# Optimization experiments

Hardware: AMD Instinct MI355X
Metric: run time of the kernel (lower is better)

Reference implementation:

```python
import jax, jax.numpy as jnp
import numpy as np
import math

T, N, P, H, E, S, R = 64, 1024, 256, 256, 512, 16, 16

def _sincos(n, d):
    pos = np.arange(n)[:, None].astype(np.float32)
    div = np.exp(np.arange(0, d, 2).astype(np.float32) * -(math.log(10000.0) / d))
    pe = np.zeros((n, d), np.float32)
    pe[:, 0::2] = np.sin(pos * div)
    pe[:, 1::2] = np.cos(pos * div)
    return jnp.asarray(pe)

def setup_inputs():
    key = jax.random.key(0)
    ks = iter(jax.random.split(key, 40))
    def w(shape, s=0.05):
        return jax.random.normal(next(ks), shape, jnp.float32) * s
    adj_seq = (jax.random.uniform(next(ks), (T, N, N)) < 0.05).astype(jnp.float32)
    return dict(
        adj_seq=adj_seq,
        pos_emb=_sincos(N, P),
        g1_Wm=w((P, H)), g1_bm=jnp.zeros((H,), jnp.float32),
        g1_Wq=w((H, H)), g1_Wk=w((H, H)), g1_gb=jnp.asarray(-1.0, jnp.float32),
        g1_Wu=w((P + H, H)), g1_bu=jnp.zeros((H,), jnp.float32),
        g1_lg=jnp.ones((H,), jnp.float32), g1_lb=jnp.zeros((H,), jnp.float32),
        g2_Wm=w((H, H)), g2_bm=jnp.zeros((H,), jnp.float32),
        g2_Wu=w((2 * H, H)), g2_bu=jnp.zeros((H,), jnp.float32),
        g2_lg=jnp.ones((H,), jnp.float32), g2_lb=jnp.zeros((H,), jnp.float32),
        m_lg=jnp.ones((H,), jnp.float32), m_lb=jnp.zeros((H,), jnp.float32),
        m_Win=w((H, 2 * E)), m_bin=jnp.zeros((2 * E,), jnp.float32),
        m_Wdelta=w((E, R)), m_bdelta=jnp.zeros((R,), jnp.float32),
        m_Wdt=w((R, E)), m_bdt=jnp.zeros((E,), jnp.float32),
        m_WB=w((E, S)), m_bB=jnp.zeros((S,), jnp.float32),
        m_WC=w((E, S)), m_bC=jnp.zeros((S,), jnp.float32),
        m_Alog=-jnp.exp(w((E, S), 0.1)),
        m_D=jnp.zeros((E,), jnp.float32),
        m_Wout=w((E, H)), m_bout=jnp.zeros((H,), jnp.float32),
    )

def _ln(x, g, b):
    mu = x.mean(-1, keepdims=True)
    v = ((x - mu) ** 2).mean(-1, keepdims=True)
    return (x - mu) / jnp.sqrt(v + 1e-5) * g + b

def reference(adj_seq, pos_emb, g1_Wm, g1_bm, g1_Wq, g1_Wk, g1_gb, g1_Wu, g1_bu,
              g1_lg, g1_lb, g2_Wm, g2_bm, g2_Wu, g2_bu, g2_lg, g2_lb,
              m_lg, m_lb, m_Win, m_bin, m_Wdelta, m_bdelta, m_Wdt, m_bdt,
              m_WB, m_bB, m_WC, m_bC, m_Alog, m_D, m_Wout, m_bout):
    scale = math.sqrt(H) * max(1.0, 1e-6)  # sqrt(d) * gate_temperature

    def encode(adj):  # adj: [N,N]
        msgs = pos_emb @ g1_Wm + g1_bm                 # [N,H]
        q = msgs @ g1_Wq
        k = msgs @ g1_Wk
        gates = jax.nn.sigmoid(q @ k.T / scale + g1_gb)
        agg = (gates * adj) @ msgs                     # gated aggregation
        x = _ln(jax.nn.relu(jnp.concatenate([pos_emb, agg], -1) @ g1_Wu + g1_bu), g1_lg, g1_lb)
        msgs2 = x @ g2_Wm + g2_bm
        agg2 = adj @ msgs2                             # ungated layer 2
        x = _ln(jax.nn.relu(jnp.concatenate([x, agg2], -1) @ g2_Wu + g2_bu), g2_lg, g2_lb)
        return x                                       # [N,H]

    seq = jax.vmap(encode)(adj_seq)                    # [T,N,H]
    x = seq.transpose(1, 0, 2)                         # [N,T,H] node-batched sequences

    # --- MambaBlock ---
    res = x
    xn = _ln(x, m_lg, m_lb)
    xp = xn @ m_Win + m_bin
    u, gate = jnp.split(xp, 2, axis=-1)                # [N,T,E] each
    u = jax.nn.silu(u)
    delta = jax.nn.softplus((u @ m_Wdelta + m_bdelta) @ m_Wdt + m_bdt)  # [N,T,E]
    Bm = u @ m_WB + m_bB                               # [N,T,S]
    Cm = u @ m_WC + m_bC                               # [N,T,S]
    A = -jnp.exp(m_Alog)                               # [E,S]

    def step(h, inp):
        u_t, d_t, B_t, C_t = inp                       # [N,E],[N,E],[N,S],[N,S]
        Ad = jnp.exp(d_t[:, :, None] * A[None])        # [N,E,S]
        h = Ad * h + d_t[:, :, None] * B_t[:, None, :] * u_t[:, :, None]
        y = jnp.einsum('ns,nes->ne', C_t, h)
        return h, y

    h0 = jnp.zeros((N, E, S), x.dtype)
    _, ys = jax.lax.scan(step, h0, (u.transpose(1, 0, 2), delta.transpose(1, 0, 2),
                                    Bm.transpose(1, 0, 2), Cm.transpose(1, 0, 2)))
    y = ys.transpose(1, 0, 2)                          # [N,T,E]
    y = (y + u * m_D) * jax.nn.silu(gate)
    out = y @ m_Wout + m_bout + res                    # [N,T,H]
    return out.transpose(1, 0, 2)                      # [T,N,H]
```

## Files before the change

### kernel.cpp

```cpp
#include <hip/hip_runtime.h>
#include <hip/hip_bf16.h>

typedef __hip_bfloat16 bf16;
typedef __attribute__((ext_vector_type(8))) short s16x8;
typedef __attribute__((ext_vector_type(4))) short s16x4;
typedef __attribute__((ext_vector_type(4))) float f32x4;

#define TT 64
#define NN_ 1024
#define EE 512

__device__ __forceinline__ float toF(float v) { return v; }
__device__ __forceinline__ float toF(bf16 v) { return __bfloat162float(v); }
__device__ __forceinline__ bf16 f2b(float v) { return __float2bfloat16(v); }

#if __has_builtin(__builtin_amdgcn_exp2f)
#define EXP2F(x) __builtin_amdgcn_exp2f(x)
#else
#define EXP2F(x) exp2f(x)
#endif
#if __has_builtin(__builtin_amdgcn_logf)
#define LOG2F(x) __builtin_amdgcn_logf(x)
#else
#define LOG2F(x) log2f(x)
#endif

enum { EPI_F32 = 0, EPI_SIG_F32 = 1, EPI_SIG_B16 = 2 };
enum { E_LN1 = 0, E_BF16 = 1, E_LN2 = 2, E_SILU = 3, E_OUT = 4, E_TRI = 5, E_BF16T = 6 };

template <bool TRANSB, int EPI>
__global__ __launch_bounds__(256) void gemm_k(
    const float* __restrict__ A, const float* __restrict__ B,
    float* __restrict__ outF, const float* __restrict__ bias,
    const float* __restrict__ sbeta, float alpha,
    int M, int Nn, int K, int lda, int ldb)
{
    __shared__ float As[16][68];
    __shared__ float Bs[16][68];
    const int tid = threadIdx.x;
    const int tx = tid & 15, ty = tid >> 4;
    const int m0 = blockIdx.x * 64, n0 = blockIdx.y * 64;
    float acc[4][4] = {};

    for (int k0 = 0; k0 < K; k0 += 16) {
        {
            int row = tid >> 2, kk0 = (tid & 3) * 4, grow = m0 + row;
#pragma unroll
            for (int j = 0; j < 4; j++) {
                int kk = kk0 + j, gk = k0 + kk;
                As[kk][row] = (grow < M) ? A[(size_t)grow * lda + gk] : 0.f;
            }
        }
        if (!TRANSB) {
            int kk = tid >> 4, c0 = (tid & 15) * 4;
#pragma unroll
            for (int j = 0; j < 4; j++) {
                int col = c0 + j, gn = n0 + col;
                Bs[kk][col] = (gn < Nn) ? B[(size_t)(k0 + kk) * ldb + gn] : 0.f;
            }
        } else {
            int col = tid >> 2, kk0 = (tid & 3) * 4, gn = n0 + col;
#pragma unroll
            for (int j = 0; j < 4; j++) {
                int kk = kk0 + j;
                Bs[kk][col] = (gn < Nn) ? B[(size_t)gn * ldb + (k0 + kk)] : 0.f;
            }
        }
        __syncthreads();
#pragma unroll
        for (int kk = 0; kk < 16; kk++) {
            float a[4], b[4];
#pragma unroll
            for (int i = 0; i < 4; i++) a[i] = As[kk][ty * 4 + i];
#pragma unroll
            for (int j = 0; j < 4; j++) b[j] = Bs[kk][tx * 4 + j];
#pragma unroll
            for (int i = 0; i < 4; i++)
#pragma unroll
                for (int j = 0; j < 4; j++)
                    acc[i][j] = fmaf(a[i], b[j], acc[i][j]);
        }
        __syncthreads();
    }

    float gb = (EPI != EPI_F32 && sbeta) ? sbeta[0] : 0.f;
#pragma unroll
    for (int i = 0; i < 4; i++) {
        int row = m0 + ty * 4 + i;
        if (row >= M) continue;
#pragma unroll
        for (int j = 0; j < 4; j++) {
            int col = n0 + tx * 4 + j;
            if (col >= Nn) continue;
            float v = acc[i][j];
            if (EPI == EPI_F32) {
                if (bias) v += bias[col];
                outF[(size_t)row * Nn + col] = v;
            } else if (EPI == EPI_SIG_F32) {
                v = v * alpha + gb;
                outF[(size_t)row * Nn + col] = 1.f / (1.f + __expf(-v));
            } else {
                v = v * alpha + gb;
                ((bf16*)outF)[(size_t)row * Nn + col] = f2b(1.f / (1.f + __expf(-v)));
            }
        }
    }
}

template <int BM, int BN, bool CAT, int EPI>
__global__ __launch_bounds__(256) void mfma_k(
    const bf16* __restrict__ A1, const bf16* __restrict__ A2, unsigned rowmask,
    const bf16* __restrict__ BT, const float* __restrict__ bias,
    float* __restrict__ outF,
    bf16* __restrict__ outB, bf16* __restrict__ outB2,
    const float* __restrict__ g1, const float* __restrict__ b1,
    const float* __restrict__ g2, const float* __restrict__ b2,
    const bf16* __restrict__ resid,
    int M, int K)
{
    constexpr bool LN = (EPI == E_LN1 || EPI == E_LN2);
    constexpr int STAGE_B = (BM * 32 + BN * 32) * 2;
    constexpr int SB = LN ? (64 * 260 * 4) : STAGE_B;
    __shared__ __align__(16) char smem[SB];
    short* As = (short*)smem;
    short* Bs = As + BM * 32;
    float* Cs = (float*)smem;

    const int tid = threadIdx.x;
    const int wid = tid >> 6, lane = tid & 63;
    const int wr = (BN == 256) ? 0 : wid;
    const int wc = (BN == 256) ? wid : 0;
    const int m0 = blockIdx.x * BM, n0 = blockIdx.y * BN;
    const int srow = tid >> 2;
    const int skoff = (tid & 3) * 8;

    f32x4 acc[4][4] = {};

    for (int k0 = 0; k0 < K; k0 += 32) {
#pragma unroll
        for (int c = 0; c < BM / 64; c++) {
            int r = c * 64 + srow;
            int gr = m0 + r;
            const bf16* p;
            if (CAT) {
                int gk = k0 + skoff;
                p = (gk < 256) ? (A1 + (size_t)(gr & rowmask) * 256 + gk)
                               : (A2 + (size_t)gr * 256 + (gk - 256));
            } else {
                p = A1 + (size_t)gr * K + k0 + skoff;
            }
            *(s16x8*)&As[r * 32 + skoff] = *(const s16x8*)p;
        }
#pragma unroll
        for (int c = 0; c < BN / 64; c++) {
            int r = c * 64 + srow;
            *(s16x8*)&Bs[r * 32 + skoff] =
                *(const s16x8*)(BT + (size_t)(n0 + r) * K + k0 + skoff);
        }
        __syncthreads();
        s16x8 af[4], bf[4];
#pragma unroll
        for (int mi = 0; mi < 4; mi++)
            af[mi] = *(s16x8*)&As[(wr * 64 + mi * 16 + (lane & 15)) * 32 + (lane >> 4) * 8];
#pragma unroll
        for (int ni = 0; ni < 4; ni++)
            bf[ni] = *(s16x8*)&Bs[(wc * 64 + ni * 16 + (lane & 15)) * 32 + (lane >> 4) * 8];
#pragma unroll
        for (int mi = 0; mi < 4; mi++)
#pragma unroll
            for (int ni = 0; ni < 4; ni++)
                acc[mi][ni] = __builtin_amdgcn_mfma_f32_16x16x32_bf16(
                    af[mi], bf[ni], acc[mi][ni], 0, 0, 0);
        __syncthreads();
    }

    if (EPI == E_SILU) {
#pragma unroll
        for (int mi = 0; mi < 4; mi++)
#pragma unroll
            for (int ni = 0; ni < 4; ni++)
#pragma unroll
                for (int r = 0; r < 4; r++) {
                    int row = m0 + wr * 64 + mi * 16 + (lane >> 4) * 4 + r;
                    int col = n0 + wc * 64 + ni * 16 + (lane & 15);
                    float v = acc[mi][ni][r] + bias[col];
                    float s = v / (1.f + __expf(-v));
                    if (col < EE) outB[(size_t)row * EE + col] = f2b(s);
                    else          outB2[(size_t)row * EE + (col - EE)] = f2b(s);
                }
    } else if (EPI == E_BF16) {
#pragma unroll
        for (int mi = 0; mi < 4; mi++)
#pragma unroll
            for (int ni = 0; ni < 4; ni++)
#pragma unroll
                for (int r = 0; r < 4; r++) {
                    int row = m0 + wr * 64 + mi * 16 + (lane >> 4) * 4 + r;
                    int col = n0 + wc * 64 + ni * 16 + (lane & 15);
                    outB[(size_t)row * 256 + col] = f2b(acc[mi][ni][r] + bias[col]);
                }
    } else if (EPI == E_BF16T) {
#pragma unroll
        for (int mi = 0; mi < 4; mi++)
#pragma unroll
            for (int ni = 0; ni < 4; ni++)
#pragma unroll
                for (int r = 0; r < 4; r++) {
                    int row = m0 + wr * 64 + mi * 16 + (lane >> 4) * 4 + r;
                    int col = n0 + wc * 64 + ni * 16 + (lane & 15);
                    size_t dst = (((size_t)(row >> 10)) * 256 + col) * 1024 + (row & 1023);
                    outB[dst] = f2b(acc[mi][ni][r] + bias[col]);
                }
    } else if (EPI == E_OUT) {
#pragma unroll
        for (int mi = 0; mi < 4; mi++)
#pragma unroll
            for (int ni = 0; ni < 4; ni++)
#pragma unroll
                for (int r = 0; r < 4; r++) {
                    int row = m0 + wr * 64 + mi * 16 + (lane >> 4) * 4 + r;
                    int col = n0 + wc * 64 + ni * 16 + (lane & 15);
                    float v = acc[mi][ni][r] + bias[col] + toF(resid[(size_t)row * 256 + col]);
                    int t = row & 63, n = row >> 6;
                    outF[((size_t)t * NN_ + n) * 256 + col] = v;
                }
    } else if (EPI == E_TRI) {
#pragma unroll
        for (int mi = 0; mi < 4; mi++)
#pragma unroll
            for (int ni = 0; ni < 4; ni++)
#pragma unroll
                for (int r = 0; r < 4; r++) {
                    int row = m0 + wid * 64 + mi * 16 + (lane >> 4) * 4 + r;
                    int col = ni * 16 + (lane & 15);
                    if (col < 48) {
                        float v = acc[mi][ni][r] + bias[col];
                        outF[(size_t)row * 48 + col] = v;
                    }
                }
    } else {
#pragma unroll
        for (int mi = 0; mi < 4; mi++)
#pragma unroll
            for (int ni = 0; ni < 4; ni++)
#pragma unroll
                for (int r = 0; r < 4; r++) {
                    int rl = mi * 16 + (lane >> 4) * 4 + r;
                    int cl = wc * 64 + ni * 16 + (lane & 15);
                    Cs[rl * 260 + cl] = fmaxf(acc[mi][ni][r] + bias[cl], 0.f);
                }
        __syncthreads();
        float g1v[4], b1v[4], g2v[4], b2v[4];
#pragma unroll
        for (int i = 0; i < 4; i++) {
            g1v[i] = g1[lane * 4 + i];
            b1v[i] = b1[lane * 4 + i];
            if (EPI == E_LN2) { g2v[i] = g2[lane * 4 + i]; b2v[i] = b2[lane * 4 + i]; }
        }
        for (int rr = 0; rr < 16; rr++) {
            int rl = wid * 16 + rr;
            int grow = m0 + rl;
            float x[4];
#pragma unroll
            for (int i = 0; i < 4; i++) x[i] = Cs[rl * 260 + lane * 4 + i];
            float s = x[0] + x[1] + x[2] + x[3];
#pragma unroll
            for (int o = 1; o < 64; o <<= 1) s += __shfl_xor(s, o, 64);
            float mu = s * (1.f / 256.f);
            float d[4], ss = 0.f;
#pragma unroll
            for (int i = 0; i < 4; i++) { d[i] = x[i] - mu; ss = fmaf(d[i], d[i], ss); }
#pragma unroll
            for (int o = 1; o < 64; o <<= 1) ss += __shfl_xor(ss, o, 64);
            float inv = rsqrtf(fmaxf(ss * (1.f / 256.f), 0.f) + 1e-5f);
            float y[4];
#pragma unroll
            for (int i = 0; i < 4; i++) y[i] = d[i] * inv * g1v[i] + b1v[i];
            if (EPI == E_LN1) {
                __align__(8) bf16 pk[4];
#pragma unroll
                for (int i = 0; i < 4; i++) pk[i] = f2b(y[i]);
                *(s16x4*)&outB[(size_t)grow * 256 + lane * 4] = *(s16x4*)pk;
            } else {
                int trow = (grow & 1023) * 64 + (grow >> 10);
                __align__(8) bf16 pk[4];
#pragma unroll
                for (int i = 0; i < 4; i++) pk[i] = f2b(y[i]);
                *(s16x4*)&outB[(size_t)trow * 256 + lane * 4] = *(s16x4*)pk;
                float s2 = y[0] + y[1] + y[2] + y[3];
#pragma unroll
                for (int o = 1; o < 64; o <<= 1) s2 += __shfl_xor(s2, o, 64);
                float mu2 = s2 * (1.f / 256.f);
                float d2[4], ss2 = 0.f;
#pragma unroll
                for (int i = 0; i < 4; i++) { d2[i] = y[i] - mu2; ss2 = fmaf(d2[i], d2[i], ss2); }
#pragma unroll
                for (int o = 1; o < 64; o <<= 1) ss2 += __shfl_xor(ss2, o, 64);
                float inv2 = rsqrtf(fmaxf(ss2 * (1.f / 256.f), 0.f) + 1e-5f);
                __align__(8) bf16 pk2[4];
#pragma unroll
                for (int i = 0; i < 4; i++) pk2[i] = f2b(d2[i] * inv2 * g2v[i] + b2v[i]);
                *(s16x4*)&outB2[(size_t)trow * 256 + lane * 4] = *(s16x4*)pk2;
            }
        }
    }
}

__global__ __launch_bounds__(256) void packadj_k(
    const float4* __restrict__ adj4, unsigned int* __restrict__ bits32)
{
    const size_t nwords = (size_t)TT * NN_ * NN_ / 32;
    const size_t stride = (size_t)gridDim.x * 256;
    for (size_t w = (size_t)blockIdx.x * 256 + threadIdx.x; w < nwords; w += stride) {
        const float4* __restrict__ p = adj4 + w * 8;
        float4 v[8];
#pragma unroll
        for (int i = 0; i < 8; i++) v[i] = p[i];
        unsigned int m = 0;
#pragma unroll
        for (int i = 0; i < 8; i++) {
            m |= (v[i].x != 0.f ? 1u : 0u) << (4 * i);
            m |= (v[i].y != 0.f ? 2u : 0u) << (4 * i);
            m |= (v[i].z != 0.f ? 4u : 0u) << (4 * i);
            m |= (v[i].w != 0.f ? 8u : 0u) << (4 * i);
        }
        bits32[w] = m;
    }
}

template <bool GATED>
__global__ __launch_bounds__(256, 2) void aggmm_k(
    const unsigned char* __restrict__ adjbits, const bf16* __restrict__ gatesb,
    const bf16* __restrict__ BTsrc, bf16* __restrict__ out)
{
    __shared__ __align__(16) short As[128 * 40];
    __shared__ __align__(16) short Bs[256 * 40];
    const int tid = threadIdx.x;
    const int wid = tid >> 6, lane = tid & 63;
    const int wr = wid & 1;
    const int wc = wid >> 1;
    const int bx = blockIdx.x;
    const int t = bx >> 3, n0 = (bx & 7) * 128;
    const int srow = tid >> 2;
    const int skoff = (tid & 3) * 8;

    const unsigned char* __restrict__ abB =
        adjbits + ((size_t)t * 1024 + n0) * 128 + (tid & 3);
    const bf16* __restrict__ gB = GATED ? (gatesb + (size_t)n0 * 1024 + skoff) : nullptr;
    const bf16* __restrict__ bt = GATED ? BTsrc : (BTsrc + (size_t)t * 256 * 1024);
    const size_t orow0 = (size_t)t * 1024 + n0;

    f32x4 acc[4][8] = {};

    unsigned char pm[2];
    s16x8 pg[2];
    s16x8 pb[4];

    auto LOADA = [&](int k0) {
#pragma unroll
        for (int c = 0; c < 2; c++) {
            int r = c * 64 + srow;
            pm[c] = abB[(size_t)r * 128 + (k0 >> 3)];
            if (GATED) pg[c] = *(const s16x8*)(gB + (size_t)r * 1024 + k0);
        }
#pragma unroll
        for (int c = 0; c < 4; c++)
            pb[c] = *(const s16x8*)(bt + (size_t)(c * 64 + srow) * 1024 + k0 + skoff);
    };
    auto STORE = [&]() {
#pragma unroll
        for (int c = 0; c < 2; c++) {
            unsigned m = pm[c];
            s16x8 tmp;
            if (GATED) {
#pragma unroll
                for (int i = 0; i < 8; i++) tmp[i] = ((m >> i) & 1) ? pg[c][i] : (short)0;
            } else {
#pragma unroll
                for (int i = 0; i < 8; i++) tmp[i] = ((m >> i) & 1) ? (short)0x3F80 : (short)0;
            }
            *(s16x8*)&As[(c * 64 + srow) * 40 + skoff] = tmp;
        }
#pragma unroll
        for (int c = 0; c < 4; c++)
            *(s16x8*)&Bs[(c * 64 + srow) * 40 + skoff] = pb[c];
    };

    LOADA(0);
#pragma unroll 1
    for (int k0 = 0; k0 < 1024; k0 += 32) {
        STORE();
        __syncthreads();
        if (k0 + 32 < 1024) LOADA(k0 + 32);
        s16x8 af[4];
#pragma unroll
        for (int mi = 0; mi < 4; mi++)
            af[mi] = *(s16x8*)&As[(wr * 64 + mi * 16 + (lane & 15)) * 40 + (lane >> 4) * 8];
#pragma unroll
        for (int ni = 0; ni < 8; ni++) {
            s16x8 bfv = *(s16x8*)&Bs[(wc * 128 + ni * 16 + (lane & 15)) * 40 + (lane >> 4) * 8];
#pragma unroll
            for (int mi = 0; mi < 4; mi++)
                acc[mi][ni] = __builtin_amdgcn_mfma_f32_16x16x32_bf16(
                    af[mi], bfv, acc[mi][ni], 0, 0, 0);
        }
        __syncthreads();
    }

#pragma unroll
    for (int mi = 0; mi < 4; mi++)
#pragma unroll
        for (int ni = 0; ni < 8; ni++)
#pragma unroll
            for (int r = 0; r < 4; r++) {
                int rowl = wr * 64 + mi * 16 + (lane >> 4) * 4 + r;
                int col = wc * 128 + ni * 16 + (lane & 15);
                out[(orow0 + rowl) * 256 + col] = f2b(acc[mi][ni][r]);
            }
}

__global__ __launch_bounds__(512) void scan_k(
    const bf16* __restrict__ u, const bf16* __restrict__ sg,
    const float* __restrict__ dbc,
    const float* __restrict__ Wdt, const float* __restrict__ bdt,
    const float* __restrict__ Alog, const float* __restrict__ D,
    bf16* __restrict__ yg)
{
    const int n = blockIdx.x, e = threadIdx.x;
    float al[16], wdt[16], h[16];
#pragma unroll
    for (int s = 0; s < 16; s++) {
        al[s] = -__expf(Alog[e * 16 + s]) * 1.44269504f;
        h[s] = 0.f;
    }
#pragma unroll
    for (int k = 0; k < 16; k++) wdt[k] = Wdt[(size_t)k * EE + e];
    const float bdte = bdt[e], De = D[e];
    const float* __restrict__ rowp = dbc + (size_t)n * TT * 48;
    const size_t base = (size_t)n * TT * EE + e;
#pragma unroll 2
    for (int t = 0; t < TT; t++) {
        const float* __restrict__ r = rowp + t * 48;
        float a0 = bdte, a1 = 0.f, a2 = 0.f, a3 = 0.f;
#pragma unroll
        for (int k = 0; k < 4; k++) {
            a0 = fmaf(r[k],      wdt[k],      a0);
            a1 = fmaf(r[k + 4],  wdt[k + 4],  a1);
            a2 = fmaf(r[k + 8],  wdt[k + 8],  a2);
            a3 = fmaf(r[k + 12], wdt[k + 12], a3);
        }
        float acc = (a0 + a1) + (a2 + a3);
        float delta = (acc > 20.f)
            ? acc
            : 0.69314718056f * LOG2F(1.f + EXP2F(acc * 1.44269504f));
        size_t idx = base + (size_t)t * EE;
        float uv = toF(u[idx]);
        float du = delta * uv;
        float y0 = 0.f, y1 = 0.f, y2 = 0.f, y3 = 0.f;
#pragma unroll
        for (int s = 0; s < 16; s += 4) {
            float ad0 = EXP2F(delta * al[s]);
            float ad1 = EXP2F(delta * al[s + 1]);
            float ad2 = EXP2F(delta * al[s + 2]);
            float ad3 = EXP2F(delta * al[s + 3]);
            h[s]     = fmaf(ad0, h[s],     du * r[16 + s]);
            h[s + 1] = fmaf(ad1, h[s + 1], du * r[17 + s]);
            h[s + 2] = fmaf(ad2, h[s + 2], du * r[18 + s]);
            h[s + 3] = fmaf(ad3, h[s + 3], du * r[19 + s]);
            y0 = fmaf(r[32 + s], h[s],     y0);
            y1 = fmaf(r[33 + s], h[s + 1], y1);
            y2 = fmaf(r[34 + s], h[s + 2], y2);
            y3 = fmaf(r[35 + s], h[s + 3], y3);
        }
        float y = (y0 + y1) + (y2 + y3);
        yg[idx] = f2b((y + uv * De) * toF(sg[idx]));
    }
}

__global__ void cast_k(const float* __restrict__ in, bf16* __restrict__ out, int n) {
    int i = blockIdx.x * 256 + threadIdx.x;
    if (i < n) out[i] = f2b(in[i]);
}
__global__ void transT_k(const float* __restrict__ W, bf16* __restrict__ out, int K, int Nn) {
    int gid = blockIdx.x * 256 + threadIdx.x;
    if (gid >= K * Nn) return;
    int n = gid / K, k = gid - n * K;
    out[gid] = f2b(W[(size_t)k * Nn + n]);
}
__global__ void transmsgs_k(const float* __restrict__ msgs, bf16* __restrict__ msgsT) {
    int gid = blockIdx.x * 256 + threadIdx.x;
    int c = gid >> 10, j = gid & 1023;
    msgsT[gid] = f2b(msgs[(size_t)j * 256 + c]);
}
__global__ void wdbct_k(const float* __restrict__ Wd, const float* __restrict__ WB,
                        const float* __restrict__ WC, bf16* __restrict__ out,
                        const float* __restrict__ bd, const float* __restrict__ bB,
                        const float* __restrict__ bC, float* __restrict__ biascat) {
    int gid = blockIdx.x * 256 + threadIdx.x;
    if (gid < 48) biascat[gid] = (gid < 16) ? bd[gid] : (gid < 32) ? bB[gid - 16] : bC[gid - 32];
    if (gid >= 64 * 512) return;
    int n = gid >> 9, k = gid & 511;
    float v = 0.f;
    if (n < 16)      v = Wd[(size_t)k * 16 + n];
    else if (n < 32) v = WB[(size_t)k * 16 + (n - 16)];
    else if (n < 48) v = WC[(size_t)k * 16 + (n - 32)];
    out[gid] = f2b(v);
}

extern "C" void kernel_launch(void* const* d_in, const int* in_sizes, int n_in,
                              void* d_out, int out_size, void* d_ws, size_t ws_size,
                              hipStream_t stream)
{
    const float* adj   = (const float*)d_in[0];
    const float* pos   = (const float*)d_in[1];
    const float* g1Wm  = (const float*)d_in[2];
    const float* g1bm  = (const float*)d_in[3];
    const float* g1Wq  = (const float*)d_in[4];
    const float* g1Wk  = (const float*)d_in[5];
    const float* g1gb  = (const float*)d_in[6];
    const float* g1Wu  = (const float*)d_in[7];
    const float* g1bu  = (const float*)d_in[8];
    const float* g1lg  = (const float*)d_in[9];
    const float* g1lb  = (const float*)d_in[10];
    const float* g2Wm  = (const float*)d_in[11];
    const float* g2bm  = (const float*)d_in[12];
    const float* g2Wu  = (const float*)d_in[13];
    const float* g2bu  = (const float*)d_in[14];
    const float* g2lg  = (const float*)d_in[15];
    const float* g2lb  = (const float*)d_in[16];
    const float* mlg   = (const float*)d_in[17];
    const float* mlb   = (const float*)d_in[18];
    const float* mWin  = (const float*)d_in[19];
    const float* mbin  = (const float*)d_in[20];
    const float* mWd   = (const float*)d_in[21];
    const float* mbd   = (const float*)d_in[22];
    const float* mWdt  = (const float*)d_in[23];
    const float* mbdt  = (const float*)d_in[24];
    const float* mWB   = (const float*)d_in[25];
    const float* mbB   = (const float*)d_in[26];
    const float* mWC   = (const float*)d_in[27];
    const float* mbC   = (const float*)d_in[28];
    const float* mAlog = (const float*)d_in[29];
    const float* mD    = (const float*)d_in[30];
    const float* mWout = (const float*)d_in[31];
    const float* mbout = (const float*)d_in[32];
    float* out = (float*)d_out;
    char* ws = (char*)d_ws;

    const size_t BIGE = (size_t)TT * NN_ * 256;
    size_t o = 0;
    auto alloc = [&](size_t bytes) { size_t r = o; o += (bytes + 255) & ~(size_t)255; return r; };

    float* msgs  = (float*)(ws + alloc((size_t)NN_ * 256 * 4));
    float* q     = (float*)(ws + alloc((size_t)NN_ * 256 * 4));
    float* kk    = (float*)(ws + alloc((size_t)NN_ * 256 * 4));
    bf16*  gatesb = (bf16*)(ws + alloc((size_t)NN_ * NN_ * 2));
    unsigned long long* adjbits =
        (unsigned long long*)(ws + alloc((size_t)TT * NN_ * NN_ / 8));
    bf16*  Ra    = (bf16*)(ws + alloc(BIGE * 2));
    size_t off_x1 = alloc(BIGE * 2);
    bf16*  x1    = (bf16*)(ws + off_x1);
    bf16*  agg2  = (bf16*)(ws + alloc(BIGE * 2));
    bf16*  x2    = (bf16*)(ws + alloc(BIGE * 2));
    bf16*  yg    = (bf16*)(ws + alloc(BIGE * 2));
    bf16*  sg    = (bf16*)(ws + alloc((size_t)NN_ * TT * EE * 2));
    float* dbc   = (float*)(ws + alloc((size_t)TT * NN_ * 48 * 4));
    bf16*  u     = (bf16*)(ws + off_x1);
    bf16* posb   = (bf16*)(ws + alloc((size_t)NN_ * 256 * 2));
    bf16* g1WuT  = (bf16*)(ws + alloc((size_t)256 * 512 * 2));
    bf16* g2WmT  = (bf16*)(ws + alloc((size_t)256 * 256 * 2));
    bf16* g2WuT  = (bf16*)(ws + alloc((size_t)256 * 512 * 2));
    bf16* mWinT  = (bf16*)(ws + alloc((size_t)1024 * 256 * 2));
    bf16* mWoutT = (bf16*)(ws + alloc((size_t)256 * 512 * 2));
    bf16* WdBCT  = (bf16*)(ws + alloc((size_t)64 * 512 * 2));
    float* biascat = (float*)(ws + alloc(64 * 4));
    bf16* msgsT  = (bf16*)(ws + alloc((size_t)256 * 1024 * 2));
    bf16* msgs2T = (bf16*)(ws + alloc(BIGE * 2));

    const unsigned ALLR = 0xFFFFFFFFu;
    const int M = TT * NN_;

    packadj_k<<<2048, 256, 0, stream>>>((const float4*)adj, (unsigned int*)adjbits);
    cast_k<<<NN_, 256, 0, stream>>>(pos, posb, NN_ * 256);
    transT_k<<<(512 * 256 + 255) / 256, 256, 0, stream>>>(g1Wu, g1WuT, 512, 256);
    transT_k<<<(256 * 256 + 255) / 256, 256, 0, stream>>>(g2Wm, g2WmT, 256, 256);
    transT_k<<<(512 * 256 + 255) / 256, 256, 0, stream>>>(g2Wu, g2WuT, 512, 256);
    transT_k<<<(256 * 1024 + 255) / 256, 256, 0, stream>>>(mWin, mWinT, 256, 1024);
    transT_k<<<(512 * 256 + 255) / 256, 256, 0, stream>>>(mWout, mWoutT, 512, 256);
    wdbct_k<<<(64 * 512 + 255) / 256, 256, 0, stream>>>(mWd, mWB, mWC, WdBCT, mbd, mbB, mbC, biascat);

    gemm_k<false, EPI_F32><<<dim3(16, 4), 256, 0, stream>>>(
        pos, g1Wm, msgs, g1bm, nullptr, 1.f, NN_, 256, 256, 256, 256);
    transmsgs_k<<<1024, 256, 0, stream>>>(msgs, msgsT);
    gemm_k<false, EPI_F32><<<dim3(16, 4), 256, 0, stream>>>(
        msgs, g1Wq, q, nullptr, nullptr, 1.f, NN_, 256, 256, 256, 256);
    gemm_k<false, EPI_F32><<<dim3(16, 4), 256, 0, stream>>>(
        msgs, g1Wk, kk, nullptr, nullptr, 1.f, NN_, 256, 256, 256, 256);
    gemm_k<true, EPI_SIG_B16><<<dim3(16, 16), 256, 0, stream>>>(
        q, kk, (float*)gatesb, nullptr, g1gb, 1.f / 16.f, NN_, NN_, 256, 256, 256);
    aggmm_k<true><<<512, 256, 0, stream>>>(
        (const unsigned char*)adjbits, gatesb, msgsT, Ra);
    mfma_k<64, 256, true, E_LN1><<<dim3(1024, 1), 256, 0, stream>>>(
        posb, Ra, 1023u, g1WuT, g1bu, nullptr, x1, nullptr,
        g1lg, g1lb, nullptr, nullptr, nullptr, M, 512);
    mfma_k<64, 256, false, E_BF16T><<<dim3(1024, 1), 256, 0, stream>>>(
        x1, x1, ALLR, g2WmT, g2bm, nullptr, msgs2T, nullptr,
        nullptr, nullptr, nullptr, nullptr, nullptr, M, 256);
    aggmm_k<false><<<512, 256, 0, stream>>>(
        (const unsigned char*)adjbits, nullptr, msgs2T, agg2);
    mfma_k<64, 256, true, E_LN2><<<dim3(1024, 1), 256, 0, stream>>>(
        x1, agg2, ALLR, g2WuT, g2bu, nullptr, x2, Ra,
        g2lg, g2lb, mlg, mlb, nullptr, M, 512);
    mfma_k<64, 256, false, E_SILU><<<dim3(1024, 4), 256, 0, stream>>>(
        Ra, Ra, ALLR, mWinT, mbin, nullptr, u, sg,
        nullptr, nullptr, nullptr, nullptr, nullptr, M, 256);
    mfma_k<256, 64, false, E_TRI><<<dim3(256, 1), 256, 0, stream>>>(
        u, u, ALLR, WdBCT, biascat, dbc, nullptr, nullptr,
        nullptr, nullptr, nullptr, nullptr, nullptr, M, 512);
    scan_k<<<NN_, 512, 0, stream>>>(u, sg, dbc, mWdt, mbdt, mAlog, mD, yg);
    mfma_k<64, 256, false, E_OUT><<<dim3(1024, 1), 256, 0, stream>>>(
        yg, yg, ALLR, mWoutT, mbout, out, nullptr, nullptr,
        nullptr, nullptr, nullptr, nullptr, x2, M, 512);

    (void)in_sizes; (void)n_in; (void)out_size; (void)ws_size;
}
```

Before: 1.075 ms.

## Prefetch GEMM tiles into registers, stage transposed stores in LDS, split scan blocks

The MFMA GEMM loop now loads the next K-tile from global memory into registers while the current tile is being computed, overlapping load latency with the MFMA work. The transposed BF16 epilogue first writes the tile to padded shared memory, then each thread writes 8 contiguous bf16 values per store along the node dimension, replacing scattered 2-byte writes. The scan kernel is split into two 256-thread blocks per node instead of one 512-thread block. The changes cost extra registers for the prefetch buffers and extra LDS for the transpose staging.

```diff
diff --git a/kernel.cpp b/kernel.cpp
--- a/kernel.cpp
+++ b/kernel.cpp
@@ -120,7 +120,8 @@
 {
     constexpr bool LN = (EPI == E_LN1 || EPI == E_LN2);
     constexpr int STAGE_B = (BM * 32 + BN * 32) * 2;
-    constexpr int SB = LN ? (64 * 260 * 4) : STAGE_B;
+    constexpr int TRB = (EPI == E_BF16T) ? (64 * 268 * 2) : 0;
+    constexpr int SB = LN ? (64 * 260 * 4) : (STAGE_B > TRB ? STAGE_B : TRB);
     __shared__ __align__(16) char smem[SB];
     short* As = (short*)smem;
     short* Bs = As + BM * 32;
@@ -135,8 +136,9 @@
     const int skoff = (tid & 3) * 8;
 
     f32x4 acc[4][4] = {};
-
-    for (int k0 = 0; k0 < K; k0 += 32) {
+    s16x8 pa[BM / 64], pbv[BN / 64];
+
+    auto LOADT = [&](int k0) {
 #pragma unroll
         for (int c = 0; c < BM / 64; c++) {
             int r = c * 64 + srow;
@@ -149,15 +151,26 @@
             } else {
                 p = A1 + (size_t)gr * K + k0 + skoff;
             }
-            *(s16x8*)&As[r * 32 + skoff] = *(const s16x8*)p;
+            pa[c] = *(const s16x8*)p;
         }
 #pragma unroll
         for (int c = 0; c < BN / 64; c++) {
             int r = c * 64 + srow;
-            *(s16x8*)&Bs[r * 32 + skoff] =
-                *(const s16x8*)(BT + (size_t)(n0 + r) * K + k0 + skoff);
-        }
-        __syncthreads();
+            pbv[c] = *(const s16x8*)(BT + (size_t)(n0 + r) * K + k0 + skoff);
+        }
+    };
+
+    LOADT(0);
+#pragma unroll 1
+    for (int k0 = 0; k0 < K; k0 += 32) {
+#pragma unroll
+        for (int c = 0; c < BM / 64; c++)
+            *(s16x8*)&As[(c * 64 + srow) * 32 + skoff] = pa[c];
+#pragma unroll
+        for (int c = 0; c < BN / 64; c++)
+            *(s16x8*)&Bs[(c * 64 + srow) * 32 + skoff] = pbv[c];
+        __syncthreads();
+        if (k0 + 32 < K) LOADT(k0 + 32);
         s16x8 af[4], bf[4];
 #pragma unroll
         for (int mi = 0; mi < 4; mi++)
@@ -200,17 +213,29 @@
                     outB[(size_t)row * 256 + col] = f2b(acc[mi][ni][r] + bias[col]);
                 }
     } else if (EPI == E_BF16T) {
+        short* Ts = (short*)smem;
 #pragma unroll
         for (int mi = 0; mi < 4; mi++)
 #pragma unroll
             for (int ni = 0; ni < 4; ni++)
 #pragma unroll
                 for (int r = 0; r < 4; r++) {
-                    int row = m0 + wr * 64 + mi * 16 + (lane >> 4) * 4 + r;
-                    int col = n0 + wc * 64 + ni * 16 + (lane & 15);
-                    size_t dst = (((size_t)(row >> 10)) * 256 + col) * 1024 + (row & 1023);
-                    outB[dst] = f2b(acc[mi][ni][r] + bias[col]);
+                    int rl = mi * 16 + (lane >> 4) * 4 + r;
+                    int cl = wc * 64 + ni * 16 + (lane & 15);
+                    union { bf16 b; short s; } u;
+                    u.b = f2b(acc[mi][ni][r] + bias[cl]);
+                    Ts[rl * 268 + cl] = u.s;
                 }
+        __syncthreads();
+        const int col = tid;
+        size_t dbase = (((size_t)(m0 >> 10)) * 256 + col) * 1024 + (m0 & 1023);
+#pragma unroll
+        for (int j0 = 0; j0 < 64; j0 += 8) {
+            s16x8 v;
+#pragma unroll
+            for (int i = 0; i < 8; i++) v[i] = Ts[(j0 + i) * 268 + col];
+            *(s16x8*)&outB[dbase + j0] = v;
+        }
     } else if (EPI == E_OUT) {
 #pragma unroll
         for (int mi = 0; mi < 4; mi++)
@@ -419,14 +444,14 @@
             }
 }
 
-__global__ __launch_bounds__(512) void scan_k(
+__global__ __launch_bounds__(256) void scan_k(
     const bf16* __restrict__ u, const bf16* __restrict__ sg,
     const float* __restrict__ dbc,
     const float* __restrict__ Wdt, const float* __restrict__ bdt,
     const float* __restrict__ Alog, const float* __restrict__ D,
     bf16* __restrict__ yg)
 {
-    const int n = blockIdx.x, e = threadIdx.x;
+    const int n = blockIdx.x, e = blockIdx.y * 256 + threadIdx.x;
     float al[16], wdt[16], h[16];
 #pragma unroll
     for (int s = 0; s < 16; s++) {
@@ -617,7 +642,7 @@
     mfma_k<256, 64, false, E_TRI><<<dim3(256, 1), 256, 0, stream>>>(
         u, u, ALLR, WdBCT, biascat, dbc, nullptr, nullptr,
         nullptr, nullptr, nullptr, nullptr, nullptr, M, 512);
-    scan_k<<<NN_, 512, 0, stream>>>(u, sg, dbc, mWdt, mbdt, mAlog, mD, yg);
+    scan_k<<<dim3(NN_, 2), 256, 0, stream>>>(u, sg, dbc, mWdt, mbdt, mAlog, mD, yg);
     mfma_k<64, 256, false, E_OUT><<<dim3(1024, 1), 256, 0, stream>>>(
         yg, yg, ALLR, mWoutT, mbout, out, nullptr, nullptr,
         nullptr, nullptr, nullptr, nullptr, x2, M, 512);
```

Result: no change. 1.063 ms (-1.1%).
